# Optimization experiments

Hardware: AMD Instinct MI355X
Metric: run time of the kernel (lower is better)

The kernel has to match this reference:

```python
import jax, jax.numpy as jnp
import numpy as np

N_OBJ, N_P, N2 = 16, 128, 2048
C, H, W = 256, 384, 384
IMG_W, IMG_H = 384.0, 384.0  # img_metas['img_shape'][:2][::-1]
SIM_THR = 0.0
LOSS_WEIGHT = 1.0
COS_EPS = 1e-8  # torch F.cosine_similarity default


def setup_inputs() -> dict:
    key = jax.random.key(0)
    k1, k2, k3, k4 = jax.random.split(key, 4)
    img_size = jnp.array([IMG_W, IMG_H], jnp.float32)
    point_set_1 = jax.random.uniform(k1, (N_OBJ, N_P, 2), jnp.float32) * img_size
    point_set_2 = jax.random.uniform(k2, (N_OBJ, N2, 2), jnp.float32) * img_size
    key_points = jax.random.uniform(k3, (N_OBJ * N_P, 2), jnp.float32) * img_size
    feats = jax.random.normal(k4, (1, C, H, W), jnp.float32)
    return {"point_set_1": point_set_1, "point_set_2": point_set_2,
            "feats": feats, "key_points": key_points}


def _grid_sample(img, pts01):
    # img: [C,H,W]; pts01: [P,2] (x,y) in [0,1]. Bilinear, align_corners=False,
    # zero padding -- matches mmcv point_sample / torch grid_sample.
    Ci, Hi, Wi = img.shape
    g = 2.0 * pts01 - 1.0
    x = ((g[:, 0] + 1.0) * Wi - 1.0) * 0.5
    y = ((g[:, 1] + 1.0) * Hi - 1.0) * 0.5
    x0 = jnp.floor(x)
    y0 = jnp.floor(y)
    wx1 = x - x0
    wy1 = y - y0

    def tap(xi, yi, wgt):
        valid = (xi >= 0) & (xi < Wi) & (yi >= 0) & (yi < Hi)
        xc = jnp.clip(xi, 0, Wi - 1).astype(jnp.int32)
        yc = jnp.clip(yi, 0, Hi - 1).astype(jnp.int32)
        return img[:, yc, xc] * (wgt * valid)[None, :]  # [C,P]

    return (tap(x0, y0, (1 - wx1) * (1 - wy1))
            + tap(x0 + 1, y0, wx1 * (1 - wy1))
            + tap(x0, y0 + 1, (1 - wx1) * wy1)
            + tap(x0 + 1, y0 + 1, wx1 * wy1))  # [C,P]


def reference(point_set_1, point_set_2, feats, key_points):
    img_size = jnp.array([IMG_W, IMG_H], feats.dtype)
    img = feats[0]  # feats.expand() reuses the same map for every object

    # feats_set_1: [n_obj, n_p, C]; feats_set_2: [n_obj, n2, C]
    f1 = _grid_sample(img, key_points / img_size).T.reshape(N_OBJ, N_P, C)
    f2 = _grid_sample(img, (point_set_2 / img_size).reshape(-1, 2)).T.reshape(N_OBJ, N2, C)

    # cosine similarity over channel dim (norms clamped to eps like torch)
    n1 = jnp.maximum(jnp.linalg.norm(f1, axis=-1), COS_EPS)  # [O,P]
    n2 = jnp.maximum(jnp.linalg.norm(f2, axis=-1), COS_EPS)  # [O,N2]
    sims = jnp.einsum('opc,onc->opn', f1, f2) / (n1[..., None] * n2[:, None, :])
    mask = sims >= SIM_THR  # [O,P,N2]

    # pairwise L2 distances between each key point and candidate set
    diff = point_set_1[:, :, None, :] - point_set_2[:, None, :, :]
    d = jnp.linalg.norm(diff, axis=-1)  # [O,P,N2]

    cnt = mask.sum(-1)  # [O,P]
    has = cnt > 0
    dmin = jnp.min(jnp.where(mask, d, jnp.inf), axis=-1)
    dmean = jnp.sum(jnp.where(mask, d, 0.0), axis=-1) / jnp.maximum(cnt, 1)
    # chamfer of a single point vs masked set: (nearest + mean)/2, 'mean' reduction
    m = (point_set_2.sum(axis=(1, 2)) >= 0).astype(d.dtype)  # [O]
    cost = jnp.where(has, 0.5 * (dmin + dmean), 0.0) * m[:, None]  # [O,P]

    dist = (cost.sum(-1) / N_P).mean()
    return dist * LOSS_WEIGHT
```

## Files before the change

### kernel.cpp

```cpp
#include <hip/hip_runtime.h>
#include <hip/hip_bf16.h>
#include <math.h>

#define W_    384
#define H_    384
#define HW_   (384*384)
#define C_    256
#define NOBJ  16
#define NP    128
#define N2    2048
#define NF1   (NOBJ*NP)
#define NPTS  (NOBJ*NP + NOBJ*N2)
#define NG    16
#define NT    8

typedef __attribute__((ext_vector_type(8))) short short8;
typedef __attribute__((ext_vector_type(4))) float f32x4;

__device__ __forceinline__ unsigned short f2bf(float v) {
    unsigned int u = __float_as_uint(v);
    u += 0x7fffu + ((u >> 16) & 1u);
    return (unsigned short)(u >> 16);
}

__device__ __forceinline__ void gload_lds16(const void* g, void* l) {
    __builtin_amdgcn_global_load_lds(
        (const __attribute__((address_space(1))) void*)g,
        (__attribute__((address_space(3))) void*)l, 16, 0, 0);
}

__global__ __launch_bounds__(256) void k_transpose(const float* __restrict__ feats,
                                                   unsigned short* __restrict__ ftT) {
    __shared__ float tile[64 * 64];
    int b     = blockIdx.x;
    int pbase = (b % (HW_ / 64)) * 64;
    int cbase = (b / (HW_ / 64)) * 64;
    int t     = threadIdx.x;
    int l     = t & 63;
    int w     = t >> 6;

    #pragma unroll
    for (int pass = 0; pass < 4; ++pass) {
        int c    = pass * 16 + w * 4 + (l >> 4);
        int psrc = ((l & 15) * 4) ^ (((c >> 3) & 3) << 3);
        const float* src = feats + (size_t)(cbase + c) * HW_ + pbase + psrc;
        float* dst = &tile[pass * 1024 + w * 256];
        gload_lds16(src, dst);
    }
    asm volatile("s_waitcnt vmcnt(0)" ::: "memory");
    __syncthreads();

    int c8  = (t & 7) * 8;
    int p0  = t >> 3;
    int swz = (t & 3) << 3;
    #pragma unroll
    for (int pass = 0; pass < 2; ++pass) {
        int p   = p0 + pass * 32;
        int psw = p ^ swz;
        unsigned short u[8];
        #pragma unroll
        for (int j = 0; j < 8; ++j) u[j] = f2bf(tile[(c8 + j) * 64 + psw]);
        uint4 pk;
        pk.x = (unsigned)u[0] | ((unsigned)u[1] << 16);
        pk.y = (unsigned)u[2] | ((unsigned)u[3] << 16);
        pk.z = (unsigned)u[4] | ((unsigned)u[5] << 16);
        pk.w = (unsigned)u[6] | ((unsigned)u[7] << 16);
        *(uint4*)(ftT + (size_t)(pbase + p) * C_ + cbase + c8) = pk;
    }
}

__global__ __launch_bounds__(256) void k_sample(const float* __restrict__ kpts,
                                                const float* __restrict__ ps2,
                                                const unsigned short* __restrict__ ftT,
                                                unsigned short* __restrict__ f12) {
    int wave  = blockIdx.x * 4 + (threadIdx.x >> 6);
    int lane  = threadIdx.x & 63;
    int half  = lane >> 5;
    int l32   = lane & 31;
    int point = wave * 2 + half;
    int cb    = l32 * 8;

    const float* src = (point < NF1) ? (kpts + (size_t)point * 2)
                                     : (ps2 + (size_t)(point - NF1) * 2);
    float x  = src[0] - 0.5f;
    float y  = src[1] - 0.5f;
    float x0 = floorf(x), y0 = floorf(y);
    int ix0 = (int)x0, iy0 = (int)y0;
    float fx = x - x0, fy = y - y0;

    float a[8] = {0.f, 0.f, 0.f, 0.f, 0.f, 0.f, 0.f, 0.f};
    #pragma unroll
    for (int dy = 0; dy < 2; ++dy) {
        #pragma unroll
        for (int dx = 0; dx < 2; ++dx) {
            int ix = ix0 + dx, iy = iy0 + dy;
            float w = (dx ? fx : 1.f - fx) * (dy ? fy : 1.f - fy);
            if (ix >= 0 && ix < W_ && iy >= 0 && iy < H_) {
                uint4 tv = *(const uint4*)(ftT + ((size_t)(iy * W_ + ix) * C_ + cb));
                a[0] += w * __uint_as_float(tv.x << 16);
                a[1] += w * __uint_as_float(tv.x & 0xffff0000u);
                a[2] += w * __uint_as_float(tv.y << 16);
                a[3] += w * __uint_as_float(tv.y & 0xffff0000u);
                a[4] += w * __uint_as_float(tv.z << 16);
                a[5] += w * __uint_as_float(tv.z & 0xffff0000u);
                a[6] += w * __uint_as_float(tv.w << 16);
                a[7] += w * __uint_as_float(tv.w & 0xffff0000u);
            }
        }
    }
    uint4 pk;
    pk.x = (unsigned)f2bf(a[0]) | ((unsigned)f2bf(a[1]) << 16);
    pk.y = (unsigned)f2bf(a[2]) | ((unsigned)f2bf(a[3]) << 16);
    pk.z = (unsigned)f2bf(a[4]) | ((unsigned)f2bf(a[5]) << 16);
    pk.w = (unsigned)f2bf(a[6]) | ((unsigned)f2bf(a[7]) << 16);
    *(uint4*)(f12 + (size_t)point * C_ + cb) = pk;
}

__global__ __launch_bounds__(256) void k_sample_direct(const float* __restrict__ kpts,
                                                       const float* __restrict__ ps2,
                                                       const float* __restrict__ feats,
                                                       unsigned short* __restrict__ f12) {
    int point = blockIdx.x * 4 + (threadIdx.x >> 6);
    int lane  = threadIdx.x & 63;
    int cb    = lane * 4;

    const float* src = (point < NF1) ? (kpts + (size_t)point * 2)
                                     : (ps2 + (size_t)(point - NF1) * 2);
    float x  = src[0] - 0.5f, y = src[1] - 0.5f;
    float x0 = floorf(x), y0 = floorf(y);
    int ix0 = (int)x0, iy0 = (int)y0;
    float fx = x - x0, fy = y - y0;

    float acc[4] = {0.f, 0.f, 0.f, 0.f};
    #pragma unroll
    for (int dy = 0; dy < 2; ++dy) {
        #pragma unroll
        for (int dx = 0; dx < 2; ++dx) {
            int ix = ix0 + dx, iy = iy0 + dy;
            float w = (dx ? fx : 1.f - fx) * (dy ? fy : 1.f - fy);
            if (ix >= 0 && ix < W_ && iy >= 0 && iy < H_) {
                int base = iy * W_ + ix;
                #pragma unroll
                for (int u = 0; u < 4; ++u)
                    acc[u] += w * feats[(size_t)(cb + u) * HW_ + base];
            }
        }
    }
    ushort4 o;
    o.x = f2bf(acc[0]); o.y = f2bf(acc[1]); o.z = f2bf(acc[2]); o.w = f2bf(acc[3]);
    *(ushort4*)(f12 + (size_t)point * C_ + cb) = o;
}

__device__ __forceinline__ void bload(const short* bbase, int t, short8* dst) {
    const short8* bp = (const short8*)(bbase + (size_t)t * 16 * C_);
    #pragma unroll
    for (int kb = 0; kb < 8; ++kb) dst[kb] = bp[kb * 4];
}

__global__ __launch_bounds__(256) void k_simdist(const unsigned short* __restrict__ f12,
                                                 const float* __restrict__ ps1,
                                                 const float* __restrict__ ps2,
                                                 float* __restrict__ pmin,
                                                 float* __restrict__ psum,
                                                 float* __restrict__ pcnt) {
    int wid  = blockIdx.x * 4 + (threadIdx.x >> 6);
    int lane = threadIdx.x & 63;
    int ng = wid & 15;
    int pt = (wid >> 4) & 7;
    int o  = wid >> 7;
    int quad = lane >> 4, col = lane & 15;

    const short* f12s = (const short*)f12;
    const short8* aptr =
        (const short8*)(f12s + ((size_t)(o * NP + pt * 16 + col) * C_ + quad * 8));
    short8 a[8];
    #pragma unroll
    for (int kb = 0; kb < 8; ++kb) a[kb] = aptr[kb * 4];

    const short* bbase = f12s + ((size_t)(NF1 + o * N2 + ng * 128 + col) * C_ + quad * 8);

    const float2* ps1v = (const float2*)ps1;
    const float2* ps2v = (const float2*)ps2;
    float pxr[4], pyr[4];
    #pragma unroll
    for (int r = 0; r < 4; ++r) {
        float2 pc = ps1v[o * NP + pt * 16 + quad * 4 + r];
        pxr[r] = pc.x; pyr[r] = pc.y;
    }

    float mn[4] = {INFINITY, INFINITY, INFINITY, INFINITY};
    float sm[4] = {0.f, 0.f, 0.f, 0.f};
    float ct[4] = {0.f, 0.f, 0.f, 0.f};

    auto ctile = [&](int t, short8 (&b)[8]) {
        f32x4 acc = {0.f, 0.f, 0.f, 0.f};
        #pragma unroll
        for (int kb = 0; kb < 8; ++kb)
            acc = __builtin_amdgcn_mfma_f32_16x16x32_bf16(a[kb], b[kb], acc, 0, 0, 0);
        float2 nc = ps2v[o * N2 + ng * 128 + t * 16 + col];
        #pragma unroll
        for (int r = 0; r < 4; ++r) {
            if (acc[r] >= 0.f) {
                float dx = pxr[r] - nc.x, dy = pyr[r] - nc.y;
                float d  = sqrtf(dx * dx + dy * dy);
                mn[r] = fminf(mn[r], d); sm[r] += d; ct[r] += 1.f;
            }
        }
    };

    short8 b0[8], b1[8];
    bload(bbase, 0, b0);
    for (int t = 0; t < NT; t += 2) {
        bload(bbase, t + 1, b1);
        ctile(t, b0);
        if (t + 2 < NT) bload(bbase, t + 2, b0);
        ctile(t + 1, b1);
    }

    #pragma unroll
    for (int r = 0; r < 4; ++r) {
        #pragma unroll
        for (int off = 1; off < 16; off <<= 1) {
            mn[r] = fminf(mn[r], __shfl_xor(mn[r], off, 16));
            sm[r] += __shfl_xor(sm[r], off, 16);
            ct[r] += __shfl_xor(ct[r], off, 16);
        }
    }
    if (col == 0) {
        #pragma unroll
        for (int r = 0; r < 4; ++r) {
            int p   = pt * 16 + quad * 4 + r;
            int idx = (o * NP + p) * NG + ng;
            pmin[idx] = mn[r]; psum[idx] = sm[r]; pcnt[idx] = ct[r];
        }
    }
}

__global__ __launch_bounds__(1024) void k_final(const float* __restrict__ pmin,
                                                const float* __restrict__ psum,
                                                const float* __restrict__ pcnt,
                                                float* __restrict__ out) {
    int t = threadIdx.x;
    float tot = 0.f;
    for (int pair = t; pair < NOBJ * NP; pair += 1024) {
        int base = pair * NG;
        const float4* pm = (const float4*)(pmin + base);
        const float4* ps = (const float4*)(psum + base);
        const float4* pc = (const float4*)(pcnt + base);
        float mn = INFINITY, sm = 0.f, ct = 0.f;
        #pragma unroll
        for (int g4 = 0; g4 < 4; ++g4) {
            float4 a = pm[g4], b = ps[g4], c = pc[g4];
            mn = fminf(mn, fminf(fminf(a.x, a.y), fminf(a.z, a.w)));
            sm += b.x + b.y + b.z + b.w;
            ct += c.x + c.y + c.z + c.w;
        }
        if (ct > 0.f) tot += 0.5f * (mn + sm / ct);
    }
    #pragma unroll
    for (int off = 32; off; off >>= 1) tot += __shfl_xor(tot, off, 64);
    __shared__ float wsum[16];
    if ((t & 63) == 0) wsum[t >> 6] = tot;
    __syncthreads();
    if (t < 64) {
        float v = (t < 16) ? wsum[t] : 0.f;
        #pragma unroll
        for (int off = 8; off; off >>= 1) v += __shfl_xor(v, off, 16);
        if (t == 0) out[0] = v * (1.0f / (NOBJ * NP));
    }
}

extern "C" void kernel_launch(void* const* d_in, const int* in_sizes, int n_in,
                              void* d_out, int out_size, void* d_ws, size_t ws_size,
                              hipStream_t stream) {
    const float* ps1   = (const float*)d_in[0];
    const float* ps2   = (const float*)d_in[1];
    const float* feats = (const float*)d_in[2];
    const float* kpts  = (const float*)d_in[3];
    float* out = (float*)d_out;

    const size_t sz_ftT  = (size_t)HW_ * C_ * sizeof(unsigned short);
    const size_t sz_f12  = (size_t)NPTS * C_ * sizeof(unsigned short);
    const size_t sz_part = (size_t)NOBJ * NP * NG * sizeof(float);

    char* ws = (char*)d_ws;
    if (ws_size >= sz_ftT + sz_f12 + 3 * sz_part) {
        unsigned short* ftT = (unsigned short*)ws;
        unsigned short* f12 = (unsigned short*)(ws + sz_ftT);
        float* pmin = (float*)(ws + sz_ftT + sz_f12);
        float* psum = (float*)(ws + sz_ftT + sz_f12 + sz_part);
        float* pcnt = (float*)(ws + sz_ftT + sz_f12 + 2 * sz_part);

        k_transpose<<<(HW_ / 64) * (C_ / 64), 256, 0, stream>>>(feats, ftT);
        k_sample<<<NPTS / 8, 256, 0, stream>>>(kpts, ps2, ftT, f12);
        k_simdist<<<NOBJ * 8 * NG / 4, 256, 0, stream>>>(f12, ps1, ps2, pmin, psum, pcnt);
        k_final<<<1, 1024, 0, stream>>>(pmin, psum, pcnt, out);
    } else {
        unsigned short* f12 = (unsigned short*)ws;
        float* pmin = (float*)(ws + sz_f12);
        float* psum = (float*)(ws + sz_f12 + sz_part);
        float* pcnt = (float*)(ws + sz_f12 + 2 * sz_part);

        k_sample_direct<<<NPTS / 4, 256, 0, stream>>>(kpts, ps2, feats, f12);
        k_simdist<<<NOBJ * 8 * NG / 4, 256, 0, stream>>>(f12, ps1, ps2, pmin, psum, pcnt);
        k_final<<<1, 1024, 0, stream>>>(pmin, psum, pcnt, out);
    }
}
```

Before: 275.4 us.

## Widen transpose tiles to 256 pixels and split final reduction across blocks

The feature-map transpose now stages a 64-channel by 256-pixel tile per block instead of 64x64. Each thread handles one pixel and writes eight 16-byte bf16 chunks, and the XOR swizzle is dropped. This gives four times fewer blocks and longer contiguous global reads, but uses 64 KB of LDS per block, which can limit occupancy, and may bring LDS bank conflicts back. The final reduction is also split into a 16-block first stage and a tiny second kernel, adding one launch in exchange for more parallel reads.

```diff
diff --git a/kernel.cpp b/kernel.cpp
--- a/kernel.cpp
+++ b/kernel.cpp
@@ -31,41 +31,36 @@
 
 __global__ __launch_bounds__(256) void k_transpose(const float* __restrict__ feats,
                                                    unsigned short* __restrict__ ftT) {
-    __shared__ float tile[64 * 64];
+    __shared__ float tile[64 * 256];
     int b     = blockIdx.x;
-    int pbase = (b % (HW_ / 64)) * 64;
-    int cbase = (b / (HW_ / 64)) * 64;
+    int pbase = (b % (HW_ / 256)) * 256;
+    int cbase = (b / (HW_ / 256)) * 64;
     int t     = threadIdx.x;
     int l     = t & 63;
     int w     = t >> 6;
 
     #pragma unroll
-    for (int pass = 0; pass < 4; ++pass) {
-        int c    = pass * 16 + w * 4 + (l >> 4);
-        int psrc = ((l & 15) * 4) ^ (((c >> 3) & 3) << 3);
-        const float* src = feats + (size_t)(cbase + c) * HW_ + pbase + psrc;
-        float* dst = &tile[pass * 1024 + w * 256];
-        gload_lds16(src, dst);
+    for (int pass = 0; pass < 16; ++pass) {
+        int c = pass * 4 + w;
+        const float* src = feats + (size_t)(cbase + c) * HW_ + pbase + l * 4;
+        gload_lds16(src, &tile[c * 256]);
     }
     asm volatile("s_waitcnt vmcnt(0)" ::: "memory");
     __syncthreads();
 
-    int c8  = (t & 7) * 8;
-    int p0  = t >> 3;
-    int swz = (t & 3) << 3;
-    #pragma unroll
-    for (int pass = 0; pass < 2; ++pass) {
-        int p   = p0 + pass * 32;
-        int psw = p ^ swz;
+    int p = t;
+    size_t obase = (size_t)(pbase + p) * C_ + cbase;
+    #pragma unroll
+    for (int ch = 0; ch < 8; ++ch) {
         unsigned short u[8];
         #pragma unroll
-        for (int j = 0; j < 8; ++j) u[j] = f2bf(tile[(c8 + j) * 64 + psw]);
+        for (int j = 0; j < 8; ++j) u[j] = f2bf(tile[(ch * 8 + j) * 256 + p]);
         uint4 pk;
         pk.x = (unsigned)u[0] | ((unsigned)u[1] << 16);
         pk.y = (unsigned)u[2] | ((unsigned)u[3] << 16);
         pk.z = (unsigned)u[4] | ((unsigned)u[5] << 16);
         pk.w = (unsigned)u[6] | ((unsigned)u[7] << 16);
-        *(uint4*)(ftT + (size_t)(pbase + p) * C_ + cbase + c8) = pk;
+        *(uint4*)(ftT + obase + ch * 8) = pk;
     }
 }
 
@@ -236,13 +231,16 @@
     }
 }
 
-__global__ __launch_bounds__(1024) void k_final(const float* __restrict__ pmin,
-                                                const float* __restrict__ psum,
-                                                const float* __restrict__ pcnt,
-                                                float* __restrict__ out) {
-    int t = threadIdx.x;
+__global__ __launch_bounds__(64) void k_final1(const float* __restrict__ pmin,
+                                               const float* __restrict__ psum,
+                                               const float* __restrict__ pcnt,
+                                               float* __restrict__ wpart) {
+    int b    = blockIdx.x;
+    int lane = threadIdx.x;
     float tot = 0.f;
-    for (int pair = t; pair < NOBJ * NP; pair += 1024) {
+    #pragma unroll
+    for (int rep = 0; rep < 2; ++rep) {
+        int pair = b * 64 + lane + rep * 1024;
         int base = pair * NG;
         const float4* pm = (const float4*)(pmin + base);
         const float4* ps = (const float4*)(psum + base);
@@ -250,24 +248,25 @@
         float mn = INFINITY, sm = 0.f, ct = 0.f;
         #pragma unroll
         for (int g4 = 0; g4 < 4; ++g4) {
-            float4 a = pm[g4], b = ps[g4], c = pc[g4];
+            float4 a = pm[g4], bb = ps[g4], c = pc[g4];
             mn = fminf(mn, fminf(fminf(a.x, a.y), fminf(a.z, a.w)));
-            sm += b.x + b.y + b.z + b.w;
+            sm += bb.x + bb.y + bb.z + bb.w;
             ct += c.x + c.y + c.z + c.w;
         }
         if (ct > 0.f) tot += 0.5f * (mn + sm / ct);
     }
     #pragma unroll
     for (int off = 32; off; off >>= 1) tot += __shfl_xor(tot, off, 64);
-    __shared__ float wsum[16];
-    if ((t & 63) == 0) wsum[t >> 6] = tot;
-    __syncthreads();
-    if (t < 64) {
-        float v = (t < 16) ? wsum[t] : 0.f;
-        #pragma unroll
-        for (int off = 8; off; off >>= 1) v += __shfl_xor(v, off, 16);
-        if (t == 0) out[0] = v * (1.0f / (NOBJ * NP));
-    }
+    if (lane == 0) wpart[b] = tot;
+}
+
+__global__ __launch_bounds__(64) void k_final2(const float* __restrict__ wpart,
+                                               float* __restrict__ out) {
+    int t = threadIdx.x;
+    float v = (t < 16) ? wpart[t] : 0.f;
+    #pragma unroll
+    for (int off = 8; off; off >>= 1) v += __shfl_xor(v, off, 16);
+    if (t == 0) out[0] = v * (1.0f / (NOBJ * NP));
 }
 
 extern "C" void kernel_launch(void* const* d_in, const int* in_sizes, int n_in,
@@ -282,27 +281,32 @@
     const size_t sz_ftT  = (size_t)HW_ * C_ * sizeof(unsigned short);
     const size_t sz_f12  = (size_t)NPTS * C_ * sizeof(unsigned short);
     const size_t sz_part = (size_t)NOBJ * NP * NG * sizeof(float);
+    const size_t sz_wp   = 64 * sizeof(float);
 
     char* ws = (char*)d_ws;
-    if (ws_size >= sz_ftT + sz_f12 + 3 * sz_part) {
+    if (ws_size >= sz_ftT + sz_f12 + 3 * sz_part + sz_wp) {
         unsigned short* ftT = (unsigned short*)ws;
         unsigned short* f12 = (unsigned short*)(ws + sz_ftT);
-        float* pmin = (float*)(ws + sz_ftT + sz_f12);
-        float* psum = (float*)(ws + sz_ftT + sz_f12 + sz_part);
-        float* pcnt = (float*)(ws + sz_ftT + sz_f12 + 2 * sz_part);
-
-        k_transpose<<<(HW_ / 64) * (C_ / 64), 256, 0, stream>>>(feats, ftT);
+        float* pmin  = (float*)(ws + sz_ftT + sz_f12);
+        float* psum  = (float*)(ws + sz_ftT + sz_f12 + sz_part);
+        float* pcnt  = (float*)(ws + sz_ftT + sz_f12 + 2 * sz_part);
+        float* wpart = (float*)(ws + sz_ftT + sz_f12 + 3 * sz_part);
+
+        k_transpose<<<(HW_ / 256) * (C_ / 64), 256, 0, stream>>>(feats, ftT);
         k_sample<<<NPTS / 8, 256, 0, stream>>>(kpts, ps2, ftT, f12);
         k_simdist<<<NOBJ * 8 * NG / 4, 256, 0, stream>>>(f12, ps1, ps2, pmin, psum, pcnt);
-        k_final<<<1, 1024, 0, stream>>>(pmin, psum, pcnt, out);
+        k_final1<<<16, 64, 0, stream>>>(pmin, psum, pcnt, wpart);
+        k_final2<<<1, 64, 0, stream>>>(wpart, out);
     } else {
         unsigned short* f12 = (unsigned short*)ws;
-        float* pmin = (float*)(ws + sz_f12);
-        float* psum = (float*)(ws + sz_f12 + sz_part);
-        float* pcnt = (float*)(ws + sz_f12 + 2 * sz_part);
+        float* pmin  = (float*)(ws + sz_f12);
+        float* psum  = (float*)(ws + sz_f12 + sz_part);
+        float* pcnt  = (float*)(ws + sz_f12 + 2 * sz_part);
+        float* wpart = (float*)(ws + sz_f12 + 3 * sz_part);
 
         k_sample_direct<<<NPTS / 4, 256, 0, stream>>>(kpts, ps2, feats, f12);
         k_simdist<<<NOBJ * 8 * NG / 4, 256, 0, stream>>>(f12, ps1, ps2, pmin, psum, pcnt);
-        k_final<<<1, 1024, 0, stream>>>(pmin, psum, pcnt, out);
-    }
-}
+        k_final1<<<16, 64, 0, stream>>>(pmin, psum, pcnt, wpart);
+        k_final2<<<1, 64, 0, stream>>>(wpart, out);
+    }
+}
```

Result: slower. 285.2 us (+3.6%).
